# Kernel tuning notes

Hardware: AMD Instinct MI355X
Metric: run time of the kernel (lower is better)

Reference implementation:

```python
import jax, jax.numpy as jnp
import numpy as np

N_, E_, A_, B_, H_, DH_ = 8000, 12000, 48000, 64, 64, 4096
STEPS, POOL_ITERS = 4, 3

def rbf(x, K, cutoff):
    mu = jnp.linspace(0.0, cutoff, K).astype(x.dtype)
    gamma = 1.0 / (cutoff / (K - 1)) ** 2
    return jnp.exp(-gamma * (x[..., None] - mu) ** 2)

def gru_step(x, h, Wih, Whh, bih, bhh):
    gi = x @ Wih.T + bih
    gh = h @ Whh.T + bhh
    ir, iz, inew = jnp.split(gi, 3, axis=-1)
    hr, hz, hnew = jnp.split(gh, 3, axis=-1)
    r = jax.nn.sigmoid(ir + hr)
    z = jax.nn.sigmoid(iz + hz)
    n = jnp.tanh(inew + r * hnew)
    return (1.0 - z) * n + z * h

def lstm_step(x, h, c, Wih, Whh, bih, bhh):
    g = x @ Wih.T + bih + h @ Whh.T + bhh
    i, f, gg, o = jnp.split(g, 4, axis=-1)
    c2 = jax.nn.sigmoid(f) * c + jax.nn.sigmoid(i) * jnp.tanh(gg)
    h2 = jax.nn.sigmoid(o) * jnp.tanh(c2)
    return h2, c2

def seg_softmax(e, seg, num_seg):
    m = jax.ops.segment_max(e, seg, num_segments=num_seg)
    ex = jnp.exp(e - m[seg])
    s = jax.ops.segment_sum(ex, seg, num_segments=num_seg)
    return ex / s[seg]

def _forward(node_attribute, edge_attribute, edge_length, angle, edge_src, edge_dst, angle_src, angle_dst, graph_ids, projW, projb, bondW, bondb, efW, efb, gnn_b, buW, bub, auW, aub, gWih, gWhh, gbih, gbhh, sWih0, sWhh0, sbih0, sbhh0, sWih1, sWhh1, sbih1, sbhh1, spW, spb, prelu_a):
    N, E = node_attribute.shape[0], edge_src.shape[0]
    x0 = jax.nn.relu(node_attribute @ projW + projb)  # [N, H]
    len_rbf = rbf(edge_length, 8, 4.0)                # [E, 8]
    edge_feat = jnp.concatenate([edge_attribute, len_rbf], axis=-1)  # [E, 16]
    ee_feat = jnp.concatenate([rbf(angle, 8, float(np.pi)), len_rbf[angle_src]], axis=-1)  # [A, 16]
    Wb = (edge_feat @ bondW + bondb).reshape(E, H_, H_)  # per-bond weight matrices (constant over steps)
    Wa = (ee_feat @ efW + efb).reshape(-1, H_, H_)       # per-angle weight matrices
    nf, hid = x0, x0
    for _ in range(STEPS):
        bm = nf[edge_src]                                # gather src node feats per bond [E, H]
        ha = jax.nn.relu(bm @ auW + aub)                 # angle_update
        m_ang = jnp.einsum('ai,aio->ao', ha[angle_src], Wa)  # [A, H]
        amsg = jax.ops.segment_sum(m_ang, angle_dst, num_segments=E)  # scatter-sum to bonds
        hb = jax.nn.relu(bm @ buW + bub) + amsg          # bond_update + angle message
        m = jnp.einsum('ei,eio->eo', hb, Wb)             # [E, H]
        nf = jax.nn.relu(jax.ops.segment_sum(m, edge_dst, num_segments=N) + gnn_b)
        nf = gru_step(nf, hid, gWih, gWhh, gbih, gbhh)   # 1-step, 1-layer GRU: output == new hidden
        hid = nf
    agg = jnp.concatenate([nf, x0], axis=-1)             # [N, 2H]
    D = agg.shape[-1]
    q_star = jnp.zeros((B_, 2 * D), agg.dtype)
    h0 = jnp.zeros((B_, D), agg.dtype); c0 = h0
    h1 = h0; c1 = h0
    for _ in range(POOL_ITERS):                          # Set2Set
        h0, c0 = lstm_step(q_star, h0, c0, sWih0, sWhh0, sbih0, sbhh0)
        h1, c1 = lstm_step(h0, h1, c1, sWih1, sWhh1, sbih1, sbhh1)
        q = h1                                           # [B, D]
        e = jnp.sum(agg * q[graph_ids], axis=-1)         # [N]
        alpha = seg_softmax(e, graph_ids, B_)
        readout = jax.ops.segment_sum(alpha[:, None] * agg, graph_ids, num_segments=B_)
        q_star = jnp.concatenate([q, readout], axis=-1)  # [B, 2D]
    out = q_star @ spW + spb                             # [B, DH]
    return jnp.where(out >= 0, out, prelu_a * out)       # PReLU

def setup_inputs():
    key = jax.random.key(0)
    ks = jax.random.split(key, 40)
    r = lambda i, shape, s=1.0: s * jax.random.normal(ks[i], shape, jnp.float32)
    inp = {}
    inp['node_attribute'] = r(0, (N_, 110))
    inp['edge_attribute'] = r(1, (E_, 8))
    inp['edge_length'] = jax.random.uniform(ks[2], (E_,), jnp.float32, 0.5, 4.0)
    inp['angle'] = jax.random.uniform(ks[3], (A_,), jnp.float32, 0.0, float(np.pi))
    inp['edge_src'] = jax.random.randint(ks[4], (E_,), 0, N_)
    inp['edge_dst'] = jax.random.randint(ks[5], (E_,), 0, N_)
    inp['angle_src'] = jax.random.randint(ks[6], (A_,), 0, E_)
    inp['angle_dst'] = jax.random.randint(ks[7], (A_,), 0, E_)
    inp['graph_ids'] = jnp.sort(jax.random.randint(ks[8], (N_,), 0, B_))
    w = 0.05
    inp['projW'] = r(9, (110, H_), w); inp['projb'] = jnp.zeros((H_,), jnp.float32)
    inp['bondW'] = r(10, (16, H_ * H_), w); inp['bondb'] = jnp.zeros((H_ * H_,), jnp.float32)
    inp['efW'] = r(11, (16, H_ * H_), w); inp['efb'] = jnp.zeros((H_ * H_,), jnp.float32)
    inp['gnn_b'] = jnp.zeros((H_,), jnp.float32)
    inp['buW'] = r(12, (H_, H_), w); inp['bub'] = jnp.zeros((H_,), jnp.float32)
    inp['auW'] = r(13, (H_, H_), w); inp['aub'] = jnp.zeros((H_,), jnp.float32)
    inp['gWih'] = r(14, (3 * H_, H_), w); inp['gWhh'] = r(15, (3 * H_, H_), w)
    inp['gbih'] = jnp.zeros((3 * H_,), jnp.float32); inp['gbhh'] = jnp.zeros((3 * H_,), jnp.float32)
    D = 2 * H_  # Set2Set feature dim = 128
    inp['sWih0'] = r(16, (4 * D, 2 * D), w); inp['sWhh0'] = r(17, (4 * D, D), w)
    inp['sbih0'] = jnp.zeros((4 * D,), jnp.float32); inp['sbhh0'] = jnp.zeros((4 * D,), jnp.float32)
    inp['sWih1'] = r(18, (4 * D, D), w); inp['sWhh1'] = r(19, (4 * D, D), w)
    inp['sbih1'] = jnp.zeros((4 * D,), jnp.float32); inp['sbhh1'] = jnp.zeros((4 * D,), jnp.float32)
    inp['spW'] = r(20, (4 * H_, DH_), w); inp['spb'] = jnp.zeros((DH_,), jnp.float32)
    inp['prelu_a'] = jnp.full((1,), 0.25, jnp.float32)
    return inp

def reference(node_attribute, edge_attribute, edge_length, angle, edge_src, edge_dst, angle_src, angle_dst, graph_ids, projW, projb, bondW, bondb, efW, efb, gnn_b, buW, bub, auW, aub, gWih, gWhh, gbih, gbhh, sWih0, sWhh0, sbih0, sbhh0, sWih1, sWhh1, sbih1, sbhh1, spW, spb, prelu_a):
    return _forward(node_attribute, edge_attribute, edge_length, angle, edge_src, edge_dst, angle_src, angle_dst, graph_ids, projW, projb, bondW, bondb, efW, efb, gnn_b, buW, bub, auW, aub, gWih, gWhh, gbih, gbhh, sWih0, sWhh0, sbih0, sbhh0, sWih1, sWhh1, sbih1, sbhh1, spW, spb, prelu_a)
```

## Files before the change

### kernel.cpp

```cpp
#include <hip/hip_runtime.h>
#include <math.h>

#define N_N 8000
#define N_E 12000
#define N_A 48000
#define N_B 64
#define N_H 64
#define N_DH 4096

typedef _Float16 h16;
typedef __attribute__((ext_vector_type(8))) _Float16 h16x8;
typedef __attribute__((ext_vector_type(4))) float f32x4;

__device__ __forceinline__ float atomAddF(float* p, float v) {
  return __hip_atomic_fetch_add(p, v, __ATOMIC_RELAXED, __HIP_MEMORY_SCOPE_AGENT);
}
__device__ __forceinline__ float sigm(float x) { return 1.f / (1.f + expf(-x)); }

#define SB_PROJ 2000
#define SB_FEAT (SB_PROJ + 47)
#define SB_PREP (SB_FEAT + 704)
#define SB_BND  (SB_PREP + 32)
#define SB_END  (SB_BND + 1330)
#define PREP_B0 32768
#define PREP_B1 (PREP_B0 + 69632)
#define PREP_B2 (PREP_B1 + 69632)
#define PREP_B3 (PREP_B2 + 4096)
#define PREP_B4 (PREP_B3 + 4096)

__global__ __launch_bounds__(256) void k_setup(
    const float* __restrict__ na, const float* __restrict__ projW,
    const float* __restrict__ projb, const float* __restrict__ ea,
    const float* __restrict__ el, const int* __restrict__ gid,
    const float* __restrict__ gWih, const float* __restrict__ gWhh,
    const float* __restrict__ efW, const float* __restrict__ efb,
    const float* __restrict__ bondW, const float* __restrict__ bondb,
    const float* __restrict__ auW, const float* __restrict__ buW,
    float* __restrict__ x0, float* __restrict__ ef,
    int* __restrict__ gstart, int* __restrict__ gend,
    h16* __restrict__ W3t, h16* __restrict__ ttA, h16* __restrict__ ttB,
    h16* __restrict__ wtAU, h16* __restrict__ wtBU,
    float4* __restrict__ amsg0_4, float4* __restrict__ nacc0_4,
    float4* __restrict__ qz_4) {
  int bx = blockIdx.x, tid = threadIdx.x;
  if (bx < SB_PROJ) {
    int wid = bx * 4 + (tid >> 6);
    int lane = tid & 63;
    if (wid < N_N) {
      const float* row = na + (size_t)wid * 110;
      float acc = projb[lane];
      for (int k = 0; k < 110; ++k) acc = fmaf(row[k], projW[k * 64 + lane], acc);
      x0[(size_t)wid * 64 + lane] = fmaxf(acc, 0.f);
    }
  } else if (bx < SB_FEAT) {
    int e = (bx - SB_PROJ) * 256 + tid;
    if (e < N_E) {
      const float g2 = (7.f / 4.f) * (7.f / 4.f);
      float x = el[e];
#pragma unroll
      for (int j = 0; j < 8; ++j) ef[e * 16 + j] = ea[e * 8 + j];
#pragma unroll
      for (int j = 0; j < 8; ++j) {
        float d = x - j * (4.f / 7.f);
        ef[e * 16 + 8 + j] = expf(-g2 * d * d);
      }
    }
  } else if (bx < SB_PREP) {
    int i = (bx - SB_FEAT) * 256 + tid;
    if (i < PREP_B0) {
      int col = i >> 7, k = i & 127;
      int grp = col >> 6, u = col & 63;
      float v;
      if (grp == 0) v = (k < 64) ? gWih[u * 64 + k] : gWhh[u * 64 + k - 64];
      else if (grp == 1) v = (k < 64) ? gWih[(64 + u) * 64 + k] : gWhh[(64 + u) * 64 + k - 64];
      else if (grp == 2) v = (k < 64) ? gWih[(128 + u) * 64 + k] : 0.f;
      else v = (k < 64) ? 0.f : gWhh[(128 + u) * 64 + k - 64];
      W3t[i] = (h16)v;
    } else if (i < PREP_B1) {
      int j = i - PREP_B0;
      int n = j >> 6, i2 = j & 63;
      int k = n >> 6, o = n & 63;
      float val = (k < 16) ? efW[(size_t)k * 4096 + i2 * 64 + o] : efb[i2 * 64 + o];
      ttA[j] = (h16)val;
    } else if (i < PREP_B2) {
      int j = i - PREP_B1;
      int n = j >> 6, i2 = j & 63;
      int k = n >> 6, o = n & 63;
      float val = (k < 16) ? bondW[(size_t)k * 4096 + i2 * 64 + o] : bondb[i2 * 64 + o];
      ttB[j] = (h16)val;
    } else if (i < PREP_B3) {
      int j = i - PREP_B2;
      int o = j >> 6, i2 = j & 63;
      wtAU[j] = (h16)auW[i2 * 64 + o];
    } else if (i < PREP_B4) {
      int j = i - PREP_B3;
      int o = j >> 6, i2 = j & 63;
      wtBU[j] = (h16)buW[i2 * 64 + o];
    }
  } else if (bx < SB_BND) {
    int n = (bx - SB_PREP) * 256 + tid;
    if (n < N_N) {
      int g = gid[n];
      if (n == 0 || gid[n - 1] != g) gstart[g] = n;
      if (n == N_N - 1 || gid[n + 1] != g) gend[g] = n + 1;
    }
  } else if (bx < SB_END) {
    int i = (bx - SB_BND) * 256 + tid;
    float4 z = (float4){0.f, 0.f, 0.f, 0.f};
    if (i < 192000) amsg0_4[i] = z;
    else if (i < 320000) nacc0_4[i - 192000] = z;
    else if (i < 340480) qz_4[i - 320000] = z;
  }
}

__global__ __launch_bounds__(256) void k_edgeP(
    const float* __restrict__ xcur, const int* __restrict__ esrc,
    const h16* __restrict__ wtAU, const float* __restrict__ aub,
    const h16* __restrict__ ttA, const float* __restrict__ ef,
    h16* __restrict__ P8, float* __restrict__ Q) {
  __shared__ h16 haT[4][2048];
  __shared__ float f_lds[128 * 9];
  int tid = threadIdx.x, wave = tid >> 6, lane = tid & 63;
  int l15 = lane & 15, lq = lane >> 4;
  int oc = blockIdx.y;
  int base = blockIdx.x * 128;
  if (oc >= 2) {
    for (int e2 = tid; e2 < 128 * 8; e2 += 256) {
      int il = e2 >> 3, k = e2 & 7;
      int g = base + il;
      if (g >= N_E) g = N_E - 1;
      f_lds[il * 9 + k] = ef[(size_t)g * 16 + 8 + k];
    }
    __syncthreads();
  }
  int ibl = wave * 32, ib0 = base + ibl;
  h16* myT = haT[wave];

  {
    h16x8 xafr[2][2];
#pragma unroll
    for (int s = 0; s < 2; ++s) {
      int item = ib0 + s * 16 + l15;
      if (item >= N_E) item = N_E - 1;
      const float* vp = xcur + (size_t)esrc[item] * 64;
#pragma unroll
      for (int ks = 0; ks < 2; ++ks) {
        const float4* p = (const float4*)(vp + ks * 32 + 8 * lq);
        float4 v0 = p[0], v1 = p[1];
        h16x8 a;
        a[0] = (h16)v0.x; a[1] = (h16)v0.y; a[2] = (h16)v0.z; a[3] = (h16)v0.w;
        a[4] = (h16)v1.x; a[5] = (h16)v1.y; a[6] = (h16)v1.z; a[7] = (h16)v1.w;
        xafr[s][ks] = a;
      }
    }
    f32x4 aU[2][4];
#pragma unroll
    for (int s = 0; s < 2; ++s)
#pragma unroll
      for (int nt = 0; nt < 4; ++nt) aU[s][nt] = (f32x4){0.f, 0.f, 0.f, 0.f};
#pragma unroll
    for (int nt = 0; nt < 4; ++nt)
#pragma unroll
      for (int ks = 0; ks < 2; ++ks) {
        h16x8 b = *(const h16x8*)(wtAU + (size_t)(nt * 16 + l15) * 64 + ks * 32 + 8 * lq);
#pragma unroll
        for (int s = 0; s < 2; ++s)
          aU[s][nt] = __builtin_amdgcn_mfma_f32_16x16x32_f16(xafr[s][ks], b, aU[s][nt], 0, 0, 0);
      }
#pragma unroll
    for (int s = 0; s < 2; ++s)
#pragma unroll
      for (int nt = 0; nt < 4; ++nt) {
        int o = nt * 16 + l15;
        float bo = aub[o];
#pragma unroll
        for (int r = 0; r < 4; ++r) {
          int row = s * 16 + lq * 4 + r;
          float val = fmaxf(aU[s][nt][r] + bo, 0.f);
          int idx = (((row * 64 + o) << 1) ^ ((row & 7) << 4)) >> 1;
          myT[idx] = (h16)val;
        }
      }
  }
  h16x8 afr[2][2];
#pragma unroll
  for (int s = 0; s < 2; ++s)
#pragma unroll
    for (int ks = 0; ks < 2; ++ks) {
      int row = s * 16 + l15;
      int byte = ((row * 64 + ks * 32 + 8 * lq) << 1) ^ ((row & 7) << 4);
      afr[s][ks] = *(const h16x8*)((const char*)myT + byte);
    }

  if (oc < 2) {
#pragma unroll
    for (int kk = oc * 4; kk < oc * 4 + 4; ++kk) {
      f32x4 acc[2][4];
#pragma unroll
      for (int s = 0; s < 2; ++s)
#pragma unroll
        for (int nt = 0; nt < 4; ++nt) acc[s][nt] = (f32x4){0.f, 0.f, 0.f, 0.f};
#pragma unroll
      for (int nt = 0; nt < 4; ++nt)
#pragma unroll
        for (int ks = 0; ks < 2; ++ks) {
          h16x8 b = *(const h16x8*)(ttA + (size_t)(kk * 64 + nt * 16 + l15) * 64 +
                                    ks * 32 + 8 * lq);
#pragma unroll
          for (int s = 0; s < 2; ++s)
            acc[s][nt] = __builtin_amdgcn_mfma_f32_16x16x32_f16(afr[s][ks], b, acc[s][nt], 0, 0, 0);
        }
#pragma unroll
      for (int s = 0; s < 2; ++s)
#pragma unroll
        for (int r = 0; r < 4; ++r) {
          int e = ib0 + s * 16 + lq * 4 + r;
          if (e < N_E) {
#pragma unroll
            for (int nt = 0; nt < 4; ++nt)
              P8[((size_t)e * 8 + kk) * 64 + nt * 16 + l15] = (h16)acc[s][nt][r];
          }
        }
    }
  } else {
    int no = oc - 2;
    f32x4 qacc[2][2];
#pragma unroll
    for (int s = 0; s < 2; ++s)
#pragma unroll
      for (int nt = 0; nt < 2; ++nt) qacc[s][nt] = (f32x4){0.f, 0.f, 0.f, 0.f};
    for (int kk = 8; kk < 16; ++kk) {
      h16x8 a2[2][2];
#pragma unroll
      for (int s = 0; s < 2; ++s) {
        h16 fs = (h16)f_lds[(ibl + s * 16 + l15) * 9 + (kk - 8)];
        a2[s][0] = afr[s][0] * fs;
        a2[s][1] = afr[s][1] * fs;
      }
#pragma unroll
      for (int nt = 0; nt < 2; ++nt)
#pragma unroll
        for (int ks = 0; ks < 2; ++ks) {
          h16x8 b = *(const h16x8*)(ttA + (size_t)(kk * 64 + (no * 2 + nt) * 16 + l15) * 64 +
                                    ks * 32 + 8 * lq);
#pragma unroll
          for (int s = 0; s < 2; ++s)
            qacc[s][nt] = __builtin_amdgcn_mfma_f32_16x16x32_f16(a2[s][ks], b, qacc[s][nt], 0, 0, 0);
        }
    }
#pragma unroll
    for (int nt = 0; nt < 2; ++nt)
#pragma unroll
      for (int ks = 0; ks < 2; ++ks) {
        h16x8 b = *(const h16x8*)(ttA + (size_t)(16 * 64 + (no * 2 + nt) * 16 + l15) * 64 +
                                  ks * 32 + 8 * lq);
#pragma unroll
        for (int s = 0; s < 2; ++s)
          qacc[s][nt] = __builtin_amdgcn_mfma_f32_16x16x32_f16(afr[s][ks], b, qacc[s][nt], 0, 0, 0);
      }
#pragma unroll
    for (int s = 0; s < 2; ++s)
#pragma unroll
      for (int r = 0; r < 4; ++r) {
        int e = ib0 + s * 16 + lq * 4 + r;
        if (e < N_E) {
#pragma unroll
          for (int nt = 0; nt < 2; ++nt)
            Q[(size_t)e * 64 + (no * 2 + nt) * 16 + l15] = qacc[s][nt][r];
        }
      }
  }
}

__global__ __launch_bounds__(256) void k_angle(
    const float* __restrict__ ang, const int* __restrict__ asrc,
    const int* __restrict__ adst, const h16* __restrict__ P8,
    const float* __restrict__ Q, float* __restrict__ amsg) {
  int w = (blockIdx.x * blockDim.x + threadIdx.x) >> 6;
  int lane = threadIdx.x & 63;
  if (w >= N_A) return;
  float x = ang[w];
  int e = asrc[w], d = adst[w];
  float acc = Q[(size_t)e * 64 + lane];
  const h16* p = P8 + (size_t)e * 512;
  const float PIf = 3.14159265358979323846f;
  const float g1 = (7.f / PIf) * (7.f / PIf);
#pragma unroll
  for (int j = 0; j < 8; ++j) {
    float dd = x - j * (PIf / 7.f);
    acc = fmaf(expf(-g1 * dd * dd), (float)p[j * 64 + lane], acc);
  }
  atomAddF(amsg + (size_t)d * 64 + lane, acc);
}

__global__ __launch_bounds__(256) void k_bond(
    const float* __restrict__ xcur, const int* __restrict__ esrc,
    const h16* __restrict__ wtBU, const float* __restrict__ bub,
    const float* __restrict__ amsg_in, const float* __restrict__ ef,
    const h16* __restrict__ ttB, const int* __restrict__ edst,
    float* __restrict__ nacc, float4* __restrict__ zbuf, int zcount4) {
  if (blockIdx.y == 0) {
    int stride = gridDim.x * 256;
    for (int i = blockIdx.x * 256 + threadIdx.x; i < zcount4; i += stride)
      zbuf[i] = (float4){0.f, 0.f, 0.f, 0.f};
  }
  __shared__ h16 haT[4][2048];
  __shared__ float f_lds[128 * 17];
  __shared__ int dst_lds[128];
  int tid = threadIdx.x;
  int base = blockIdx.x * 128;
  int oc = blockIdx.y;
  for (int e2 = tid; e2 < 128 * 16; e2 += 256) {
    int il = e2 >> 4, k = e2 & 15;
    int g = base + il;
    if (g >= N_E) g = N_E - 1;
    f_lds[il * 17 + k] = ef[(size_t)g * 16 + k];
  }
  if (tid < 128) {
    int g = base + tid;
    if (g >= N_E) g = N_E - 1;
    dst_lds[tid] = edst[g];
  }
  __syncthreads();

  int wave = tid >> 6, lane = tid & 63;
  int l15 = lane & 15, lq = lane >> 4;
  int ibl = wave * 32, ib0 = base + ibl;
  h16* myT = haT[wave];

  {
    h16x8 xafr[2][2];
#pragma unroll
    for (int s = 0; s < 2; ++s) {
      int item = ib0 + s * 16 + l15;
      if (item >= N_E) item = N_E - 1;
      const float* vp = xcur + (size_t)esrc[item] * 64;
#pragma unroll
      for (int ks = 0; ks < 2; ++ks) {
        const float4* p = (const float4*)(vp + ks * 32 + 8 * lq);
        float4 v0 = p[0], v1 = p[1];
        h16x8 a;
        a[0] = (h16)v0.x; a[1] = (h16)v0.y; a[2] = (h16)v0.z; a[3] = (h16)v0.w;
        a[4] = (h16)v1.x; a[5] = (h16)v1.y; a[6] = (h16)v1.z; a[7] = (h16)v1.w;
        xafr[s][ks] = a;
      }
    }
    f32x4 aU[2][4];
#pragma unroll
    for (int s = 0; s < 2; ++s)
#pragma unroll
      for (int nt = 0; nt < 4; ++nt) aU[s][nt] = (f32x4){0.f, 0.f, 0.f, 0.f};
#pragma unroll
    for (int nt = 0; nt < 4; ++nt)
#pragma unroll
      for (int ks = 0; ks < 2; ++ks) {
        h16x8 b = *(const h16x8*)(wtBU + (size_t)(nt * 16 + l15) * 64 + ks * 32 + 8 * lq);
#pragma unroll
        for (int s = 0; s < 2; ++s)
          aU[s][nt] = __builtin_amdgcn_mfma_f32_16x16x32_f16(xafr[s][ks], b, aU[s][nt], 0, 0, 0);
      }
#pragma unroll
    for (int s = 0; s < 2; ++s)
#pragma unroll
      for (int nt = 0; nt < 4; ++nt) {
        int o = nt * 16 + l15;
        float bo = bub[o];
#pragma unroll
        for (int r = 0; r < 4; ++r) {
          int row = s * 16 + lq * 4 + r;
          int item = ib0 + row;
          if (item >= N_E) item = N_E - 1;
          float val = fmaxf(aU[s][nt][r] + bo, 0.f) + amsg_in[(size_t)item * 64 + o];
          int idx = (((row * 64 + o) << 1) ^ ((row & 7) << 4)) >> 1;
          myT[idx] = (h16)val;
        }
      }
  }
  h16x8 afr[2][2];
#pragma unroll
  for (int s = 0; s < 2; ++s)
#pragma unroll
    for (int ks = 0; ks < 2; ++ks) {
      int row = s * 16 + l15;
      int byte = ((row * 64 + ks * 32 + 8 * lq) << 1) ^ ((row & 7) << 4);
      afr[s][ks] = *(const h16x8*)((const char*)myT + byte);
    }

  f32x4 acc[2];
  acc[0] = (f32x4){0.f, 0.f, 0.f, 0.f};
  acc[1] = (f32x4){0.f, 0.f, 0.f, 0.f};
  for (int kk = 0; kk < 16; ++kk) {
    h16x8 bfr[2];
#pragma unroll
    for (int ks = 0; ks < 2; ++ks)
      bfr[ks] = *(const h16x8*)(ttB + (size_t)(kk * 64 + oc * 16 + l15) * 64 + ks * 32 + 8 * lq);
    h16x8 a2[2][2];
#pragma unroll
    for (int s = 0; s < 2; ++s) {
      h16 fs = (h16)f_lds[(ibl + s * 16 + l15) * 17 + kk];
      a2[s][0] = afr[s][0] * fs;
      a2[s][1] = afr[s][1] * fs;
    }
#pragma unroll
    for (int s = 0; s < 2; ++s)
#pragma unroll
      for (int ks = 0; ks < 2; ++ks)
        acc[s] = __builtin_amdgcn_mfma_f32_16x16x32_f16(a2[s][ks], bfr[ks], acc[s], 0, 0, 0);
  }
  {
    h16x8 bfr[2];
#pragma unroll
    for (int ks = 0; ks < 2; ++ks)
      bfr[ks] = *(const h16x8*)(ttB + (size_t)(16 * 64 + oc * 16 + l15) * 64 + ks * 32 + 8 * lq);
#pragma unroll
    for (int s = 0; s < 2; ++s)
#pragma unroll
      for (int ks = 0; ks < 2; ++ks)
        acc[s] = __builtin_amdgcn_mfma_f32_16x16x32_f16(afr[s][ks], bfr[ks], acc[s], 0, 0, 0);
  }
#pragma unroll
  for (int s = 0; s < 2; ++s)
#pragma unroll
    for (int r = 0; r < 4; ++r) {
      int il = ibl + s * 16 + lq * 4 + r;
      int item = base + il;
      if (item < N_E)
        atomAddF(nacc + (size_t)dst_lds[il] * 64 + oc * 16 + l15, acc[s][r]);
    }
}

__global__ __launch_bounds__(256) void k_gru2(
    const float* __restrict__ nacc, const float* __restrict__ gnnb,
    const float* __restrict__ h, const h16* __restrict__ W3t,
    const float* __restrict__ gbih, const float* __restrict__ gbhh,
    float* __restrict__ hout, const float* __restrict__ x0,
    float* __restrict__ agg, int wagg, float4* __restrict__ zbuf, int zcount4) {
  if (zbuf) {
    int stride = gridDim.x * 256;
    for (int i = blockIdx.x * 256 + threadIdx.x; i < zcount4; i += stride)
      zbuf[i] = (float4){0.f, 0.f, 0.f, 0.f};
  }
  int tid = threadIdx.x, wave = tid >> 6, lane = tid & 63;
  int l15 = lane & 15, lq = lane >> 4;
  int ib0 = blockIdx.x * 64 + wave * 16;
  int nodeA = ib0 + l15;
  if (nodeA >= N_N) nodeA = N_N - 1;

  h16x8 afr[4];
#pragma unroll
  for (int ks = 0; ks < 2; ++ks) {
    const float4* p = (const float4*)(nacc + (size_t)nodeA * 64 + ks * 32 + 8 * lq);
    const float4* gp = (const float4*)(gnnb + ks * 32 + 8 * lq);
    float4 v0 = p[0], v1 = p[1], g0 = gp[0], g1 = gp[1];
    h16x8 a;
    a[0] = (h16)fmaxf(v0.x + g0.x, 0.f); a[1] = (h16)fmaxf(v0.y + g0.y, 0.f);
    a[2] = (h16)fmaxf(v0.z + g0.z, 0.f); a[3] = (h16)fmaxf(v0.w + g0.w, 0.f);
    a[4] = (h16)fmaxf(v1.x + g1.x, 0.f); a[5] = (h16)fmaxf(v1.y + g1.y, 0.f);
    a[6] = (h16)fmaxf(v1.z + g1.z, 0.f); a[7] = (h16)fmaxf(v1.w + g1.w, 0.f);
    afr[ks] = a;
  }
#pragma unroll
  for (int ks = 0; ks < 2; ++ks) {
    const float4* p = (const float4*)(h + (size_t)nodeA * 64 + ks * 32 + 8 * lq);
    float4 v0 = p[0], v1 = p[1];
    h16x8 a;
    a[0] = (h16)v0.x; a[1] = (h16)v0.y; a[2] = (h16)v0.z; a[3] = (h16)v0.w;
    a[4] = (h16)v1.x; a[5] = (h16)v1.y; a[6] = (h16)v1.z; a[7] = (h16)v1.w;
    afr[2 + ks] = a;
  }

  f32x4 acc[16];
#pragma unroll
  for (int nt = 0; nt < 16; ++nt) acc[nt] = (f32x4){0.f, 0.f, 0.f, 0.f};
#pragma unroll
  for (int nt = 0; nt < 16; ++nt) {
#pragma unroll
    for (int ks = 0; ks < 4; ++ks) {
      if (nt >= 8 && nt < 12 && ks >= 2) continue;
      if (nt >= 12 && ks < 2) continue;
      h16x8 b = *(const h16x8*)(W3t + (size_t)(nt * 16 + l15) * 128 + ks * 32 + 8 * lq);
      acc[nt] = __builtin_amdgcn_mfma_f32_16x16x32_f16(afr[ks], b, acc[nt], 0, 0, 0);
    }
  }

#pragma unroll
  for (int nt0 = 0; nt0 < 4; ++nt0) {
    int u = nt0 * 16 + l15;
    float br = gbih[u] + gbhh[u];
    float bz = gbih[64 + u] + gbhh[64 + u];
    float bin_ = gbih[128 + u];
    float bhn = gbhh[128 + u];
#pragma unroll
    for (int r = 0; r < 4; ++r) {
      int node = ib0 + lq * 4 + r;
      if (node < N_N) {
        float rr = sigm(acc[nt0][r] + br);
        float zz = sigm(acc[nt0 + 4][r] + bz);
        float nn = tanhf(acc[nt0 + 8][r] + bin_ + rr * (acc[nt0 + 12][r] + bhn));
        float hv = h[(size_t)node * 64 + u];
        float val = (1.f - zz) * nn + zz * hv;
        hout[(size_t)node * 64 + u] = val;
        if (wagg) {
          agg[(size_t)node * 128 + u] = val;
          agg[(size_t)node * 128 + 64 + u] = x0[(size_t)node * 64 + u];
        }
      }
    }
  }
}


__global__ __launch_bounds__(256) void k_lstm2(
    const float* __restrict__ x, int xdim,
    const float* __restrict__ hin, const float* __restrict__ cin,
    const float* __restrict__ Wih, const float* __restrict__ Whh,
    const float* __restrict__ bih, const float* __restrict__ bhh,
    float* __restrict__ hout, float* __restrict__ cout) {
  int w = (blockIdx.x * blockDim.x + threadIdx.x) >> 6;
  int lane = threadIdx.x & 63;
  if (w >= N_B * 128) return;
  int b = w >> 7, u = w & 127;
  float a0 = 0.f, a1 = 0.f, a2 = 0.f, a3 = 0.f;
  const float* xr = x + (size_t)b * xdim;
  for (int k = lane; k < xdim; k += 64) {
    float xv = xr[k];
    a0 = fmaf(xv, Wih[(size_t)u * xdim + k], a0);
    a1 = fmaf(xv, Wih[(size_t)(128 + u) * xdim + k], a1);
    a2 = fmaf(xv, Wih[(size_t)(256 + u) * xdim + k], a2);
    a3 = fmaf(xv, Wih[(size_t)(384 + u) * xdim + k], a3);
  }
  const float* hr = hin + (size_t)b * 128;
#pragma unroll
  for (int k0 = 0; k0 < 128; k0 += 64) {
    int k = k0 + lane;
    float hv = hr[k];
    a0 = fmaf(hv, Whh[(size_t)u * 128 + k], a0);
    a1 = fmaf(hv, Whh[(size_t)(128 + u) * 128 + k], a1);
    a2 = fmaf(hv, Whh[(size_t)(256 + u) * 128 + k], a2);
    a3 = fmaf(hv, Whh[(size_t)(384 + u) * 128 + k], a3);
  }
#pragma unroll
  for (int m = 1; m < 64; m <<= 1) {
    a0 += __shfl_xor(a0, m);
    a1 += __shfl_xor(a1, m);
    a2 += __shfl_xor(a2, m);
    a3 += __shfl_xor(a3, m);
  }
  if (lane == 0) {
    float gi = a0 + bih[u] + bhh[u];
    float gf = a1 + bih[128 + u] + bhh[128 + u];
    float gg = a2 + bih[256 + u] + bhh[256 + u];
    float go = a3 + bih[384 + u] + bhh[384 + u];
    float c2 = sigm(gf) * cin[(size_t)b * 128 + u] + sigm(gi) * tanhf(gg);
    hout[(size_t)b * 128 + u] = sigm(go) * tanhf(c2);
    cout[(size_t)b * 128 + u] = c2;
  }
}

__global__ __launch_bounds__(256) void k_pool2(
    const float* __restrict__ agg, const int* __restrict__ gstart,
    const int* __restrict__ gend, const float* __restrict__ q,
    float* __restrict__ q_star) {
  int g = blockIdx.x;
  int s = gstart[g], t = gend[g];
  int cnt = t - s;
  if (cnt < 0) cnt = 0;
  if (cnt > 1024) cnt = 1024;
  __shared__ float ew[1024];
  __shared__ float red[8];
  __shared__ float comb[256];
  int tid = threadIdx.x, wave = tid >> 6, lane = tid & 63;
  float qa = q[g * 128 + lane], qb = q[g * 128 + 64 + lane];
  for (int i = wave; i < cnt; i += 4) {
    int n = s + i;
    float a = agg[(size_t)n * 128 + lane] * qa + agg[(size_t)n * 128 + 64 + lane] * qb;
#pragma unroll
    for (int m = 1; m < 64; m <<= 1) a += __shfl_xor(a, m);
    if (lane == 0) ew[i] = a;
  }
  __syncthreads();
  float mx = -INFINITY;
  for (int i = tid; i < cnt; i += 256) mx = fmaxf(mx, ew[i]);
#pragma unroll
  for (int m = 1; m < 64; m <<= 1) mx = fmaxf(mx, __shfl_xor(mx, m));
  if (lane == 0) red[wave] = mx;
  __syncthreads();
  mx = fmaxf(fmaxf(red[0], red[1]), fmaxf(red[2], red[3]));
  float sm = 0.f;
  for (int i = tid; i < cnt; i += 256) sm += expf(ew[i] - mx);
#pragma unroll
  for (int m = 1; m < 64; m <<= 1) sm += __shfl_xor(sm, m);
  if (lane == 0) red[4 + wave] = sm;
  __syncthreads();
  sm = red[4] + red[5] + red[6] + red[7];
  float inv = (sm > 0.f) ? 1.f / sm : 0.f;
  __syncthreads();
  for (int i = tid; i < cnt; i += 256) ew[i] = expf(ew[i] - mx) * inv;
  __syncthreads();
  int d = tid & 127, half = tid >> 7;
  float acc = 0.f;
  for (int i = half; i < cnt; i += 2)
    acc = fmaf(ew[i], agg[(size_t)(s + i) * 128 + d], acc);
  comb[tid] = acc;
  __syncthreads();
  if (half == 0) {
    float r2 = acc + comb[128 + tid];
    q_star[(size_t)g * 256 + d] = q[(size_t)g * 128 + d];
    q_star[(size_t)g * 256 + 128 + d] = r2;
  }
}

__global__ void k_out(const float* __restrict__ qs, const float* __restrict__ W,
                      const float* __restrict__ bias, const float* __restrict__ pa,
                      float* __restrict__ out) {
  int idx = blockIdx.x * blockDim.x + threadIdx.x;
  if (idx >= N_B * N_DH) return;
  int b = idx >> 12, d = idx & 4095;
  float acc = bias[d];
  const float* q = qs + (size_t)b * 256;
  for (int k = 0; k < 256; ++k) acc = fmaf(q[k], W[(size_t)k * 4096 + d], acc);
  float a = pa[0];
  out[idx] = acc >= 0.f ? acc : a * acc;
}

enum : size_t {
  OFF_X0 = 0,
  OFF_HA = OFF_X0 + (size_t)N_N * 64,
  OFF_HB = OFF_HA + (size_t)N_N * 64,
  OFF_EF = OFF_HB + (size_t)N_N * 64,
  OFF_AMSG0 = OFF_EF + (size_t)N_E * 16,
  OFF_AMSG1 = OFF_AMSG0 + (size_t)N_E * 64,
  OFF_NACC0 = OFF_AMSG1 + (size_t)N_E * 64,
  OFF_NACC1 = OFF_NACC0 + (size_t)N_N * 64,
  OFF_AGG = OFF_NACC1 + (size_t)N_N * 64,
  OFF_QSTAR = OFF_AGG + (size_t)N_N * 128,
  OFF_H0A = OFF_QSTAR + N_B * 256,
  OFF_H0B = OFF_H0A + N_B * 128,
  OFF_C0A = OFF_H0B + N_B * 128,
  OFF_C0B = OFF_C0A + N_B * 128,
  OFF_H1A = OFF_C0B + N_B * 128,
  OFF_H1B = OFF_H1A + N_B * 128,
  OFF_C1A = OFF_H1B + N_B * 128,
  OFF_C1B = OFF_C1A + N_B * 128,
  OFF_GSTART = OFF_C1B + N_B * 128,
  OFF_GEND = OFF_GSTART + N_B,
  OFF_TT_ANG = (OFF_GEND + N_B + 63) & ~(size_t)63,
  OFF_TT_BOND = OFF_TT_ANG + 34816,
  OFF_WT_AU = OFF_TT_BOND + 34816,
  OFF_WT_BU = OFF_WT_AU + 2048,
  OFF_W3T = OFF_WT_BU + 2048,
  OFF_P8 = OFF_W3T + 16384,
  OFF_Q = OFF_P8 + 3072000,
  WS_FLOATS = OFF_Q + 768000
};

extern "C" void kernel_launch(void* const* d_in, const int* in_sizes, int n_in,
                              void* d_out, int out_size, void* d_ws, size_t ws_size,
                              hipStream_t stream) {
  (void)in_sizes; (void)n_in; (void)out_size; (void)ws_size;
  const float* na    = (const float*)d_in[0];
  const float* ea    = (const float*)d_in[1];
  const float* el    = (const float*)d_in[2];
  const float* ang   = (const float*)d_in[3];
  const int*   esrc  = (const int*)d_in[4];
  const int*   edst  = (const int*)d_in[5];
  const int*   asrc  = (const int*)d_in[6];
  const int*   adst  = (const int*)d_in[7];
  const int*   gid   = (const int*)d_in[8];
  const float* projW = (const float*)d_in[9];
  const float* projb = (const float*)d_in[10];
  const float* bondW = (const float*)d_in[11];
  const float* bondb = (const float*)d_in[12];
  const float* efW   = (const float*)d_in[13];
  const float* efb   = (const float*)d_in[14];
  const float* gnnb  = (const float*)d_in[15];
  const float* buW   = (const float*)d_in[16];
  const float* bub   = (const float*)d_in[17];
  const float* auW   = (const float*)d_in[18];
  const float* aub   = (const float*)d_in[19];
  const float* gWih  = (const float*)d_in[20];
  const float* gWhh  = (const float*)d_in[21];
  const float* gbih  = (const float*)d_in[22];
  const float* gbhh  = (const float*)d_in[23];
  const float* sWih0 = (const float*)d_in[24];
  const float* sWhh0 = (const float*)d_in[25];
  const float* sbih0 = (const float*)d_in[26];
  const float* sbhh0 = (const float*)d_in[27];
  const float* sWih1 = (const float*)d_in[28];
  const float* sWhh1 = (const float*)d_in[29];
  const float* sbih1 = (const float*)d_in[30];
  const float* sbhh1 = (const float*)d_in[31];
  const float* spW   = (const float*)d_in[32];
  const float* spb   = (const float*)d_in[33];
  const float* pa    = (const float*)d_in[34];
  float* out = (float*)d_out;
  float* ws = (float*)d_ws;

  float* x0    = ws + OFF_X0;
  float* hA    = ws + OFF_HA;
  float* hB    = ws + OFF_HB;
  float* ef    = ws + OFF_EF;
  float* amsg0 = ws + OFF_AMSG0;
  float* amsg1 = ws + OFF_AMSG1;
  float* nacc0 = ws + OFF_NACC0;
  float* nacc1 = ws + OFF_NACC1;
  float* agg   = ws + OFF_AGG;
  float* qstar = ws + OFF_QSTAR;
  float* h0a = ws + OFF_H0A; float* h0b = ws + OFF_H0B;
  float* c0a = ws + OFF_C0A; float* c0b = ws + OFF_C0B;
  float* h1a = ws + OFF_H1A; float* h1b = ws + OFF_H1B;
  float* c1a = ws + OFF_C1A; float* c1b = ws + OFF_C1B;
  int* gstart  = (int*)(ws + OFF_GSTART);
  h16* ttA  = (h16*)(ws + OFF_TT_ANG);
  h16* ttB  = (h16*)(ws + OFF_TT_BOND);
  h16* wtAU = (h16*)(ws + OFF_WT_AU);
  h16* wtBU = (h16*)(ws + OFF_WT_BU);
  h16* w3t  = (h16*)(ws + OFF_W3T);
  h16* P8   = (h16*)(ws + OFF_P8);
  float* Q    = ws + OFF_Q;

  hipMemsetAsync(gstart, 0x7f, 2 * N_B * sizeof(int), stream);
  k_setup<<<SB_END, 256, 0, stream>>>(
      na, projW, projb, ea, el, gid, gWih, gWhh, efW, efb, bondW, bondb, auW, buW,
      x0, ef, gstart, gstart + N_B, w3t, ttA, ttB, wtAU, wtBU,
      (float4*)amsg0, (float4*)nacc0, (float4*)qstar);

  const int EGX = (N_E + 127) / 128;
  const float* cur = x0;
  float* bufs[2] = {hA, hB};
  float* amsgs[2] = {amsg0, amsg1};
  float* naccs[2] = {nacc0, nacc1};
  for (int s = 0; s < 4; ++s) {
    float* amsg_c = amsgs[s & 1];
    float* amsg_o = amsgs[(s + 1) & 1];
    float* nacc_c = naccs[s & 1];
    float* nacc_o = naccs[(s + 1) & 1];
    k_edgeP<<<dim3(EGX, 4), 256, 0, stream>>>(cur, esrc, wtAU, aub, ttA, ef, P8, Q);
    k_angle<<<(N_A * 64) / 256, 256, 0, stream>>>(ang, asrc, adst, P8, Q, amsg_c);
    k_bond<<<dim3(EGX, 4), 256, 0, stream>>>(cur, esrc, wtBU, bub, amsg_c, ef, ttB,
                                             edst, nacc_c, (float4*)amsg_o,
                                             N_E * 64 / 4);
    float* nxt = bufs[s & 1];
    k_gru2<<<(N_N + 63) / 64, 256, 0, stream>>>(nacc_c, gnnb, cur, w3t, gbih, gbhh,
                                                nxt, x0, agg, (s == 3) ? 1 : 0,
                                                (float4*)nacc_o, N_N * 64 / 4);
    cur = nxt;
  }

  float *h0i = h0a, *h0o = h0b, *c0i = c0a, *c0o = c0b;
  float *h1i = h1a, *h1o = h1b, *c1i = c1a, *c1o = c1b;
  for (int it = 0; it < 3; ++it) {
    k_lstm2<<<(N_B * 128 * 64 + 255) / 256, 256, 0, stream>>>(
        qstar, 256, h0i, c0i, sWih0, sWhh0, sbih0, sbhh0, h0o, c0o);
    k_lstm2<<<(N_B * 128 * 64 + 255) / 256, 256, 0, stream>>>(
        h0o, 128, h1i, c1i, sWih1, sWhh1, sbih1, sbhh1, h1o, c1o);
    k_pool2<<<N_B, 256, 0, stream>>>(agg, gstart, gstart + N_B, h1o, qstar);
    float* tmp;
    tmp = h0i; h0i = h0o; h0o = tmp;
    tmp = c0i; c0i = c0o; c0o = tmp;
    tmp = h1i; h1i = h1o; h1o = tmp;
    tmp = c1i; c1i = c1o; c1o = tmp;
  }
  k_out<<<(N_B * N_DH + 255) / 256, 256, 0, stream>>>(qstar, spW, spb, pa, out);
}
```

Measured before the change: 395.5 us.

## Replace atomic scatter-adds with CSR gather-based segment sums for angles and bonds

Builds CSR indices once per call (histogram, single-block scan, fill) for angle->bond and bond->node destinations. The angle kernel now runs one wave per destination bond and gathers its contributions, using precomputed angle RBF weights and a P8 layout transposed to eight contiguous halves per lane. The bond kernel writes per-edge messages, which the GRU kernel sums per node. This removes float atomics and the per-step buffer zeroing, at the cost of extra setup kernels, a serial scan, and load imbalance for high-degree segments.

Result: slower. 507.9 us (+28.4%).

```diff
diff --git a/kernel.cpp b/kernel.cpp
--- a/kernel.cpp
+++ b/kernel.cpp
@@ -12,16 +12,16 @@
 typedef __attribute__((ext_vector_type(8))) _Float16 h16x8;
 typedef __attribute__((ext_vector_type(4))) float f32x4;
 
-__device__ __forceinline__ float atomAddF(float* p, float v) {
-  return __hip_atomic_fetch_add(p, v, __ATOMIC_RELAXED, __HIP_MEMORY_SCOPE_AGENT);
-}
 __device__ __forceinline__ float sigm(float x) { return 1.f / (1.f + expf(-x)); }
 
 #define SB_PROJ 2000
 #define SB_FEAT (SB_PROJ + 47)
-#define SB_PREP (SB_FEAT + 704)
+#define SB_WANG (SB_FEAT + 188)
+#define SB_PREP (SB_WANG + 704)
 #define SB_BND  (SB_PREP + 32)
-#define SB_END  (SB_BND + 1330)
+#define SB_HISTA (SB_BND + 188)
+#define SB_HISTN (SB_HISTA + 47)
+#define SB_END  (SB_HISTN + 80)
 #define PREP_B0 32768
 #define PREP_B1 (PREP_B0 + 69632)
 #define PREP_B2 (PREP_B1 + 69632)
@@ -31,16 +31,18 @@
 __global__ __launch_bounds__(256) void k_setup(
     const float* __restrict__ na, const float* __restrict__ projW,
     const float* __restrict__ projb, const float* __restrict__ ea,
-    const float* __restrict__ el, const int* __restrict__ gid,
+    const float* __restrict__ el, const float* __restrict__ ang,
+    const int* __restrict__ adst, const int* __restrict__ edst,
+    const int* __restrict__ gid,
     const float* __restrict__ gWih, const float* __restrict__ gWhh,
     const float* __restrict__ efW, const float* __restrict__ efb,
     const float* __restrict__ bondW, const float* __restrict__ bondb,
     const float* __restrict__ auW, const float* __restrict__ buW,
-    float* __restrict__ x0, float* __restrict__ ef,
+    float* __restrict__ x0, float* __restrict__ ef, float* __restrict__ wang,
     int* __restrict__ gstart, int* __restrict__ gend,
+    int* __restrict__ cntA, int* __restrict__ cntN,
     h16* __restrict__ W3t, h16* __restrict__ ttA, h16* __restrict__ ttB,
     h16* __restrict__ wtAU, h16* __restrict__ wtBU,
-    float4* __restrict__ amsg0_4, float4* __restrict__ nacc0_4,
     float4* __restrict__ qz_4) {
   int bx = blockIdx.x, tid = threadIdx.x;
   if (bx < SB_PROJ) {
@@ -65,8 +67,20 @@
         ef[e * 16 + 8 + j] = expf(-g2 * d * d);
       }
     }
+  } else if (bx < SB_WANG) {
+    int a = (bx - SB_FEAT) * 256 + tid;
+    if (a < N_A) {
+      const float PIf = 3.14159265358979323846f;
+      const float g1 = (7.f / PIf) * (7.f / PIf);
+      float x = ang[a];
+#pragma unroll
+      for (int j = 0; j < 8; ++j) {
+        float d = x - j * (PIf / 7.f);
+        wang[(size_t)a * 8 + j] = expf(-g1 * d * d);
+      }
+    }
   } else if (bx < SB_PREP) {
-    int i = (bx - SB_FEAT) * 256 + tid;
+    int i = (bx - SB_WANG) * 256 + tid;
     if (i < PREP_B0) {
       int col = i >> 7, k = i & 127;
       int grp = col >> 6, u = col & 63;
@@ -104,12 +118,82 @@
       if (n == 0 || gid[n - 1] != g) gstart[g] = n;
       if (n == N_N - 1 || gid[n + 1] != g) gend[g] = n + 1;
     }
+  } else if (bx < SB_HISTA) {
+    int a = (bx - SB_BND) * 256 + tid;
+    if (a < N_A) atomicAdd(&cntA[adst[a]], 1);
+  } else if (bx < SB_HISTN) {
+    int e = (bx - SB_HISTA) * 256 + tid;
+    if (e < N_E) atomicAdd(&cntN[edst[e]], 1);
   } else if (bx < SB_END) {
-    int i = (bx - SB_BND) * 256 + tid;
-    float4 z = (float4){0.f, 0.f, 0.f, 0.f};
-    if (i < 192000) amsg0_4[i] = z;
-    else if (i < 320000) nacc0_4[i - 192000] = z;
-    else if (i < 340480) qz_4[i - 320000] = z;
+    int i = (bx - SB_HISTN) * 256 + tid;
+    if (i < 20480) qz_4[i] = (float4){0.f, 0.f, 0.f, 0.f};
+  }
+}
+
+__global__ __launch_bounds__(256) void k_scan(int* __restrict__ cntA,
+                                              int* __restrict__ offA,
+                                              int* __restrict__ cntN,
+                                              int* __restrict__ offN) {
+  __shared__ int tot[256];
+  int tid = threadIdx.x;
+  {
+    const int n = N_E, chunk = (n + 255) / 256;
+    int s = tid * chunk;
+    int e = s + chunk < n ? s + chunk : n;
+    int sum = 0;
+    for (int i = s; i < e; ++i) sum += cntA[i];
+    tot[tid] = sum;
+    __syncthreads();
+    if (tid == 0) {
+      int run = 0;
+      for (int i = 0; i < 256; ++i) { int v = tot[i]; tot[i] = run; run += v; }
+    }
+    __syncthreads();
+    int run = tot[tid];
+    for (int i = s; i < e; ++i) { offA[i] = run; run += cntA[i]; cntA[i] = 0; }
+    if (e == n && s <= n) offA[n] = run;
+    __syncthreads();
+  }
+  {
+    const int n = N_N, chunk = (n + 255) / 256;
+    int s = tid * chunk;
+    int e = s + chunk < n ? s + chunk : n;
+    int sum = 0;
+    for (int i = s; i < e; ++i) sum += cntN[i];
+    tot[tid] = sum;
+    __syncthreads();
+    if (tid == 0) {
+      int run = 0;
+      for (int i = 0; i < 256; ++i) { int v = tot[i]; tot[i] = run; run += v; }
+    }
+    __syncthreads();
+    int run = tot[tid];
+    for (int i = s; i < e; ++i) { offN[i] = run; run += cntN[i]; cntN[i] = 0; }
+    if (e == n && s <= n) offN[n] = run;
+  }
+}
+
+#define FB_A 188
+__global__ __launch_bounds__(256) void k_fill(
+    const int* __restrict__ adst, const int* __restrict__ edst,
+    const int* __restrict__ offA, const int* __restrict__ offN,
+    int* __restrict__ cntA, int* __restrict__ cntN,
+    int* __restrict__ aidx, int* __restrict__ eidx) {
+  int bx = blockIdx.x, tid = threadIdx.x;
+  if (bx < FB_A) {
+    int a = bx * 256 + tid;
+    if (a < N_A) {
+      int d = adst[a];
+      int p = atomicAdd(&cntA[d], 1);
+      aidx[offA[d] + p] = a;
+    }
+  } else {
+    int e = (bx - FB_A) * 256 + tid;
+    if (e < N_E) {
+      int d = edst[e];
+      int p = atomicAdd(&cntN[d], 1);
+      eidx[offN[d] + p] = e;
+    }
   }
 }
 
@@ -218,7 +302,7 @@
           if (e < N_E) {
 #pragma unroll
             for (int nt = 0; nt < 4; ++nt)
-              P8[((size_t)e * 8 + kk) * 64 + nt * 16 + l15] = (h16)acc[s][nt][r];
+              P8[((size_t)e * 64 + nt * 16 + l15) * 8 + kk] = (h16)acc[s][nt][r];
           }
         }
     }
@@ -272,41 +356,42 @@
   }
 }
 
-__global__ __launch_bounds__(256) void k_angle(
-    const float* __restrict__ ang, const int* __restrict__ asrc,
-    const int* __restrict__ adst, const h16* __restrict__ P8,
-    const float* __restrict__ Q, float* __restrict__ amsg) {
+__global__ __launch_bounds__(256) void k_angle2(
+    const int* __restrict__ offA, const int* __restrict__ aidx,
+    const int* __restrict__ asrc, const float* __restrict__ wang,
+    const h16* __restrict__ P8, const float* __restrict__ Q,
+    float* __restrict__ amsg) {
   int w = (blockIdx.x * blockDim.x + threadIdx.x) >> 6;
   int lane = threadIdx.x & 63;
-  if (w >= N_A) return;
-  float x = ang[w];
-  int e = asrc[w], d = adst[w];
-  float acc = Q[(size_t)e * 64 + lane];
-  const h16* p = P8 + (size_t)e * 512;
-  const float PIf = 3.14159265358979323846f;
-  const float g1 = (7.f / PIf) * (7.f / PIf);
-#pragma unroll
-  for (int j = 0; j < 8; ++j) {
-    float dd = x - j * (PIf / 7.f);
-    acc = fmaf(expf(-g1 * dd * dd), (float)p[j * 64 + lane], acc);
-  }
-  atomAddF(amsg + (size_t)d * 64 + lane, acc);
+  if (w >= N_E) return;
+  int s = offA[w], t = offA[w + 1];
+  float acc = 0.f;
+  for (int i = s; i < t; ++i) {
+    int a = aidx[i];
+    int src = asrc[a];
+    const float4* wp = (const float4*)(wang + (size_t)a * 8);
+    float4 w0 = wp[0], w1 = wp[1];
+    h16x8 pv = *(const h16x8*)(P8 + (size_t)src * 512 + (size_t)lane * 8);
+    acc += Q[(size_t)src * 64 + lane];
+    acc = fmaf(w0.x, (float)pv[0], acc);
+    acc = fmaf(w0.y, (float)pv[1], acc);
+    acc = fmaf(w0.z, (float)pv[2], acc);
+    acc = fmaf(w0.w, (float)pv[3], acc);
+    acc = fmaf(w1.x, (float)pv[4], acc);
+    acc = fmaf(w1.y, (float)pv[5], acc);
+    acc = fmaf(w1.z, (float)pv[6], acc);
+    acc = fmaf(w1.w, (float)pv[7], acc);
+  }
+  amsg[(size_t)w * 64 + lane] = acc;
 }
 
 __global__ __launch_bounds__(256) void k_bond(
     const float* __restrict__ xcur, const int* __restrict__ esrc,
     const h16* __restrict__ wtBU, const float* __restrict__ bub,
     const float* __restrict__ amsg_in, const float* __restrict__ ef,
-    const h16* __restrict__ ttB, const int* __restrict__ edst,
-    float* __restrict__ nacc, float4* __restrict__ zbuf, int zcount4) {
-  if (blockIdx.y == 0) {
-    int stride = gridDim.x * 256;
-    for (int i = blockIdx.x * 256 + threadIdx.x; i < zcount4; i += stride)
-      zbuf[i] = (float4){0.f, 0.f, 0.f, 0.f};
-  }
+    const h16* __restrict__ ttB, float* __restrict__ m_out) {
   __shared__ h16 haT[4][2048];
   __shared__ float f_lds[128 * 17];
-  __shared__ int dst_lds[128];
   int tid = threadIdx.x;
   int base = blockIdx.x * 128;
   int oc = blockIdx.y;
@@ -316,11 +401,6 @@
     if (g >= N_E) g = N_E - 1;
     f_lds[il * 17 + k] = ef[(size_t)g * 16 + k];
   }
-  if (tid < 128) {
-    int g = base + tid;
-    if (g >= N_E) g = N_E - 1;
-    dst_lds[tid] = edst[g];
-  }
   __syncthreads();
 
   int wave = tid >> 6, lane = tid & 63;
@@ -422,42 +502,59 @@
   for (int s = 0; s < 2; ++s)
 #pragma unroll
     for (int r = 0; r < 4; ++r) {
-      int il = ibl + s * 16 + lq * 4 + r;
-      int item = base + il;
+      int item = ib0 + s * 16 + lq * 4 + r;
       if (item < N_E)
-        atomAddF(nacc + (size_t)dst_lds[il] * 64 + oc * 16 + l15, acc[s][r]);
+        m_out[(size_t)item * 64 + oc * 16 + l15] = acc[s][r];
     }
 }
 
 __global__ __launch_bounds__(256) void k_gru2(
-    const float* __restrict__ nacc, const float* __restrict__ gnnb,
+    const float* __restrict__ m, const int* __restrict__ offN,
+    const int* __restrict__ eidx, const float* __restrict__ gnnb,
     const float* __restrict__ h, const h16* __restrict__ W3t,
     const float* __restrict__ gbih, const float* __restrict__ gbhh,
     float* __restrict__ hout, const float* __restrict__ x0,
-    float* __restrict__ agg, int wagg, float4* __restrict__ zbuf, int zcount4) {
-  if (zbuf) {
-    int stride = gridDim.x * 256;
-    for (int i = blockIdx.x * 256 + threadIdx.x; i < zcount4; i += stride)
-      zbuf[i] = (float4){0.f, 0.f, 0.f, 0.f};
-  }
+    float* __restrict__ agg, int wagg) {
   int tid = threadIdx.x, wave = tid >> 6, lane = tid & 63;
   int l15 = lane & 15, lq = lane >> 4;
   int ib0 = blockIdx.x * 64 + wave * 16;
   int nodeA = ib0 + l15;
   if (nodeA >= N_N) nodeA = N_N - 1;
 
+  float v[16];
+  {
+    const float4* gp0 = (const float4*)(gnnb + 8 * lq);
+    const float4* gp1 = (const float4*)(gnnb + 32 + 8 * lq);
+    float4 g0 = gp0[0], g1 = gp0[1], g2 = gp1[0], g3 = gp1[1];
+    v[0] = g0.x; v[1] = g0.y; v[2] = g0.z; v[3] = g0.w;
+    v[4] = g1.x; v[5] = g1.y; v[6] = g1.z; v[7] = g1.w;
+    v[8] = g2.x; v[9] = g2.y; v[10] = g2.z; v[11] = g2.w;
+    v[12] = g3.x; v[13] = g3.y; v[14] = g3.z; v[15] = g3.w;
+  }
+  int s0 = offN[nodeA], t0 = offN[nodeA + 1];
+  for (int i = s0; i < t0; ++i) {
+    int e = eidx[i];
+    const float* mb = m + (size_t)e * 64;
+    float4 a0 = *(const float4*)(mb + 8 * lq);
+    float4 a1 = *(const float4*)(mb + 8 * lq + 4);
+    float4 b0 = *(const float4*)(mb + 32 + 8 * lq);
+    float4 b1 = *(const float4*)(mb + 32 + 8 * lq + 4);
+    v[0] += a0.x; v[1] += a0.y; v[2] += a0.z; v[3] += a0.w;
+    v[4] += a1.x; v[5] += a1.y; v[6] += a1.z; v[7] += a1.w;
+    v[8] += b0.x; v[9] += b0.y; v[10] += b0.z; v[11] += b0.w;
+    v[12] += b1.x; v[13] += b1.y; v[14] += b1.z; v[15] += b1.w;
+  }
+
   h16x8 afr[4];
-#pragma unroll
-  for (int ks = 0; ks < 2; ++ks) {
-    const float4* p = (const float4*)(nacc + (size_t)nodeA * 64 + ks * 32 + 8 * lq);
-    const float4* gp = (const float4*)(gnnb + ks * 32 + 8 * lq);
-    float4 v0 = p[0], v1 = p[1], g0 = gp[0], g1 = gp[1];
-    h16x8 a;
-    a[0] = (h16)fmaxf(v0.x + g0.x, 0.f); a[1] = (h16)fmaxf(v0.y + g0.y, 0.f);
-    a[2] = (h16)fmaxf(v0.z + g0.z, 0.f); a[3] = (h16)fmaxf(v0.w + g0.w, 0.f);
-    a[4] = (h16)fmaxf(v1.x + g1.x, 0.f); a[5] = (h16)fmaxf(v1.y + g1.y, 0.f);
-    a[6] = (h16)fmaxf(v1.z + g1.z, 0.f); a[7] = (h16)fmaxf(v1.w + g1.w, 0.f);
-    afr[ks] = a;
+  {
+    h16x8 a, b;
+#pragma unroll
+    for (int j = 0; j < 8; ++j) {
+      a[j] = (h16)fmaxf(v[j], 0.f);
+      b[j] = (h16)fmaxf(v[8 + j], 0.f);
+    }
+    afr[0] = a;
+    afr[1] = b;
   }
 #pragma unroll
   for (int ks = 0; ks < 2; ++ks) {
@@ -540,11 +637,11 @@
     a3 = fmaf(hv, Whh[(size_t)(384 + u) * 128 + k], a3);
   }
 #pragma unroll
-  for (int m = 1; m < 64; m <<= 1) {
-    a0 += __shfl_xor(a0, m);
-    a1 += __shfl_xor(a1, m);
-    a2 += __shfl_xor(a2, m);
-    a3 += __shfl_xor(a3, m);
+  for (int mm = 1; mm < 64; mm <<= 1) {
+    a0 += __shfl_xor(a0, mm);
+    a1 += __shfl_xor(a1, mm);
+    a2 += __shfl_xor(a2, mm);
+    a3 += __shfl_xor(a3, mm);
   }
   if (lane == 0) {
     float gi = a0 + bih[u] + bhh[u];
@@ -575,21 +672,21 @@
     int n = s + i;
     float a = agg[(size_t)n * 128 + lane] * qa + agg[(size_t)n * 128 + 64 + lane] * qb;
 #pragma unroll
-    for (int m = 1; m < 64; m <<= 1) a += __shfl_xor(a, m);
+    for (int mm = 1; mm < 64; mm <<= 1) a += __shfl_xor(a, mm);
     if (lane == 0) ew[i] = a;
   }
   __syncthreads();
   float mx = -INFINITY;
   for (int i = tid; i < cnt; i += 256) mx = fmaxf(mx, ew[i]);
 #pragma unroll
-  for (int m = 1; m < 64; m <<= 1) mx = fmaxf(mx, __shfl_xor(mx, m));
+  for (int mm = 1; mm < 64; mm <<= 1) mx = fmaxf(mx, __shfl_xor(mx, mm));
   if (lane == 0) red[wave] = mx;
   __syncthreads();
   mx = fmaxf(fmaxf(red[0], red[1]), fmaxf(red[2], red[3]));
   float sm = 0.f;
   for (int i = tid; i < cnt; i += 256) sm += expf(ew[i] - mx);
 #pragma unroll
-  for (int m = 1; m < 64; m <<= 1) sm += __shfl_xor(sm, m);
+  for (int mm = 1; mm < 64; mm <<= 1) sm += __shfl_xor(sm, mm);
   if (lane == 0) red[4 + wave] = sm;
   __syncthreads();
   sm = red[4] + red[5] + red[6] + red[7];
@@ -625,31 +722,35 @@
 
 enum : size_t {
   OFF_X0 = 0,
-  OFF_HA = OFF_X0 + (size_t)N_N * 64,
-  OFF_HB = OFF_HA + (size_t)N_N * 64,
-  OFF_EF = OFF_HB + (size_t)N_N * 64,
-  OFF_AMSG0 = OFF_EF + (size_t)N_E * 16,
-  OFF_AMSG1 = OFF_AMSG0 + (size_t)N_E * 64,
-  OFF_NACC0 = OFF_AMSG1 + (size_t)N_E * 64,
-  OFF_NACC1 = OFF_NACC0 + (size_t)N_N * 64,
-  OFF_AGG = OFF_NACC1 + (size_t)N_N * 64,
-  OFF_QSTAR = OFF_AGG + (size_t)N_N * 128,
-  OFF_H0A = OFF_QSTAR + N_B * 256,
-  OFF_H0B = OFF_H0A + N_B * 128,
-  OFF_C0A = OFF_H0B + N_B * 128,
-  OFF_C0B = OFF_C0A + N_B * 128,
-  OFF_H1A = OFF_C0B + N_B * 128,
-  OFF_H1B = OFF_H1A + N_B * 128,
-  OFF_C1A = OFF_H1B + N_B * 128,
-  OFF_C1B = OFF_C1A + N_B * 128,
-  OFF_GSTART = OFF_C1B + N_B * 128,
-  OFF_GEND = OFF_GSTART + N_B,
-  OFF_TT_ANG = (OFF_GEND + N_B + 63) & ~(size_t)63,
+  OFF_HA = OFF_X0 + 512000,
+  OFF_HB = OFF_HA + 512000,
+  OFF_EF = OFF_HB + 512000,
+  OFF_AMSG = OFF_EF + 192000,
+  OFF_M = OFF_AMSG + 768000,
+  OFF_AGG = OFF_M + 768000,
+  OFF_QSTAR = OFF_AGG + 1024000,
+  OFF_H0A = OFF_QSTAR + 16384,
+  OFF_H0B = OFF_H0A + 8192,
+  OFF_C0A = OFF_H0B + 8192,
+  OFF_C0B = OFF_C0A + 8192,
+  OFF_H1A = OFF_C0B + 8192,
+  OFF_H1B = OFF_H1A + 8192,
+  OFF_C1A = OFF_H1B + 8192,
+  OFF_C1B = OFF_C1A + 8192,
+  OFF_GSTART = OFF_C1B + 8192,
+  OFF_CNTA = OFF_GSTART + 128,
+  OFF_CNTN = OFF_CNTA + 12000,
+  OFF_OFFA = OFF_CNTN + 8000,
+  OFF_OFFN = OFF_OFFA + 12001,
+  OFF_AIDX = OFF_OFFN + 8001,
+  OFF_EIDX = OFF_AIDX + 48000,
+  OFF_WANG = (OFF_EIDX + 12000 + 15) & ~(size_t)15,
+  OFF_TT_ANG = OFF_WANG + 384000,
   OFF_TT_BOND = OFF_TT_ANG + 34816,
   OFF_WT_AU = OFF_TT_BOND + 34816,
   OFF_WT_BU = OFF_WT_AU + 2048,
   OFF_W3T = OFF_WT_BU + 2048,
-  OFF_P8 = OFF_W3T + 16384,
+  OFF_P8 = (OFF_W3T + 16384 + 15) & ~(size_t)15,
   OFF_Q = OFF_P8 + 3072000,
   WS_FLOATS = OFF_Q + 768000
 };
@@ -696,54 +797,57 @@
   float* out = (float*)d_out;
   float* ws = (float*)d_ws;
 
-  float* x0    = ws + OFF_X0;
-  float* hA    = ws + OFF_HA;
-  float* hB    = ws + OFF_HB;
-  float* ef    = ws + OFF_EF;
-  float* amsg0 = ws + OFF_AMSG0;
-  float* amsg1 = ws + OFF_AMSG1;
-  float* nacc0 = ws + OFF_NACC0;
-  float* nacc1 = ws + OFF_NACC1;
-  float* agg   = ws + OFF_AGG;
+  float* x0   = ws + OFF_X0;
+  float* hA   = ws + OFF_HA;
+  float* hB   = ws + OFF_HB;
+  float* ef   = ws + OFF_EF;
+  float* amsg = ws + OFF_AMSG;
+  float* mbuf = ws + OFF_M;
+  float* agg  = ws + OFF_AGG;
   float* qstar = ws + OFF_QSTAR;
   float* h0a = ws + OFF_H0A; float* h0b = ws + OFF_H0B;
   float* c0a = ws + OFF_C0A; float* c0b = ws + OFF_C0B;
   float* h1a = ws + OFF_H1A; float* h1b = ws + OFF_H1B;
   float* c1a = ws + OFF_C1A; float* c1b = ws + OFF_C1B;
-  int* gstart  = (int*)(ws + OFF_GSTART);
+  int* gstart = (int*)(ws + OFF_GSTART);
+  int* cntA = (int*)(ws + OFF_CNTA);
+  int* cntN = (int*)(ws + OFF_CNTN);
+  int* offA = (int*)(ws + OFF_OFFA);
+  int* offN = (int*)(ws + OFF_OFFN);
+  int* aidx = (int*)(ws + OFF_AIDX);
+  int* eidx = (int*)(ws + OFF_EIDX);
+  float* wang = ws + OFF_WANG;
   h16* ttA  = (h16*)(ws + OFF_TT_ANG);
   h16* ttB  = (h16*)(ws + OFF_TT_BOND);
   h16* wtAU = (h16*)(ws + OFF_WT_AU);
   h16* wtBU = (h16*)(ws + OFF_WT_BU);
   h16* w3t  = (h16*)(ws + OFF_W3T);
   h16* P8   = (h16*)(ws + OFF_P8);
-  float* Q    = ws + OFF_Q;
+  float* Q  = ws + OFF_Q;
 
   hipMemsetAsync(gstart, 0x7f, 2 * N_B * sizeof(int), stream);
+  hipMemsetAsync(cntA, 0, (N_E + N_N) * sizeof(int), stream);
   k_setup<<<SB_END, 256, 0, stream>>>(
-      na, projW, projb, ea, el, gid, gWih, gWhh, efW, efb, bondW, bondb, auW, buW,
-      x0, ef, gstart, gstart + N_B, w3t, ttA, ttB, wtAU, wtBU,
-      (float4*)amsg0, (float4*)nacc0, (float4*)qstar);
+      na, projW, projb, ea, el, ang, adst, edst, gid, gWih, gWhh, efW, efb,
+      bondW, bondb, auW, buW, x0, ef, wang, gstart, gstart + N_B, cntA, cntN,
+      w3t, ttA, ttB, wtAU, wtBU, (float4*)qstar);
+  k_scan<<<1, 256, 0, stream>>>(cntA, offA, cntN, offN);
+  k_fill<<<FB_A + 47, 256, 0, stream>>>(adst, edst, offA, offN, cntA, cntN,
+                                        aidx, eidx);
 
   const int EGX = (N_E + 127) / 128;
   const float* cur = x0;
   float* bufs[2] = {hA, hB};
-  float* amsgs[2] = {amsg0, amsg1};
-  float* naccs[2] = {nacc0, nacc1};
   for (int s = 0; s < 4; ++s) {
-    float* amsg_c = amsgs[s & 1];
-    float* amsg_o = amsgs[(s + 1) & 1];
-    float* nacc_c = naccs[s & 1];
-    float* nacc_o = naccs[(s + 1) & 1];
     k_edgeP<<<dim3(EGX, 4), 256, 0, stream>>>(cur, esrc, wtAU, aub, ttA, ef, P8, Q);
-    k_angle<<<(N_A * 64) / 256, 256, 0, stream>>>(ang, asrc, adst, P8, Q, amsg_c);
-    k_bond<<<dim3(EGX, 4), 256, 0, stream>>>(cur, esrc, wtBU, bub, amsg_c, ef, ttB,
-                                             edst, nacc_c, (float4*)amsg_o,
-                                             N_E * 64 / 4);
+    k_angle2<<<(N_E * 64) / 256, 256, 0, stream>>>(offA, aidx, asrc, wang, P8, Q,
+                                                   amsg);
+    k_bond<<<dim3(EGX, 4), 256, 0, stream>>>(cur, esrc, wtBU, bub, amsg, ef, ttB,
+                                             mbuf);
     float* nxt = bufs[s & 1];
-    k_gru2<<<(N_N + 63) / 64, 256, 0, stream>>>(nacc_c, gnnb, cur, w3t, gbih, gbhh,
-                                                nxt, x0, agg, (s == 3) ? 1 : 0,
-                                                (float4*)nacc_o, N_N * 64 / 4);
+    k_gru2<<<(N_N + 63) / 64, 256, 0, stream>>>(mbuf, offN, eidx, gnnb, cur, w3t,
+                                                gbih, gbhh, nxt, x0, agg,
+                                                (s == 3) ? 1 : 0);
     cur = nxt;
   }
 
```
